# Optimization experiments

Hardware: AMD Instinct MI355X
Metric: run time of the kernel (lower is better)

## Reference

```python
import jax, jax.numpy as jnp
import numpy as np

B, S, D, H = 2, 2048, 4096, 16
HD = D // H          # 256 head dim
ROT = 64             # rotary_dim
MASK_FILL = -65504.0 # fp16 min, as in the IPEX kernel


def _sinusoidal_positions(num_pos, dim):
    inv_freq = 1.0 / (10000.0 ** (np.arange(0, dim, 2, dtype=np.float32) / dim))
    sinusoid = np.einsum('i,j->ij', np.arange(num_pos, dtype=np.float32), inv_freq)
    return np.concatenate([np.sin(sinusoid), np.cos(sinusoid)], axis=-1).astype(np.float32)  # [num_pos, dim]


def setup_inputs() -> dict:
    key = jax.random.key(0)
    ks = jax.random.split(key, 6)
    w = 0.02
    return {
        'hidden_states': jax.random.normal(ks[0], (B, S, D), jnp.float32),
        'Wq': jax.random.normal(ks[1], (D, D), jnp.float32) * w,
        'Wk': jax.random.normal(ks[2], (D, D), jnp.float32) * w,
        'Wv': jax.random.normal(ks[3], (D, D), jnp.float32) * w,
        'Wo': jax.random.normal(ks[4], (D, D), jnp.float32) * w,
        'embed_positions': jnp.asarray(_sinusoidal_positions(S, ROT)),  # [max_pos, ROT] sin|cos
        'attention_mask': jnp.zeros((B, 1, 1, S), jnp.float32),
        'position_ids': jnp.tile(jnp.arange(S, dtype=jnp.int32), (B, 1)),
    }


def rotate_every_two(x):
    x1 = x[..., ::2]
    x2 = x[..., 1::2]
    return jnp.stack((-x2, x1), axis=-1).reshape(x.shape)


def reference(hidden_states, Wq, Wk, Wv, Wo, embed_positions, attention_mask, position_ids):
    b, s, d = hidden_states.shape
    q = (hidden_states @ Wq).reshape(b, s, H, HD)
    k = (hidden_states @ Wk).reshape(b, s, H, HD)
    v = (hidden_states @ Wv).reshape(b, s, H, HD)

    # gather sin/cos per position, GPT-J interleaved layout
    sincos = embed_positions[position_ids]            # [b, s, ROT]
    sin, cos = jnp.split(sincos, 2, axis=-1)          # each [b, s, ROT/2]
    sin = jnp.repeat(sin, 2, axis=-1)[:, :, None, :]  # [b, s, 1, ROT]
    cos = jnp.repeat(cos, 2, axis=-1)[:, :, None, :]

    def rope(t):
        tr = t[..., :ROT]
        tr = tr * cos + rotate_every_two(tr) * sin
        return jnp.concatenate([tr, t[..., ROT:]], axis=-1)

    q = rope(q).transpose(0, 2, 1, 3)  # [b, H, s, HD]
    k = rope(k).transpose(0, 2, 1, 3)
    v = v.transpose(0, 2, 1, 3)

    scores = jnp.einsum('bhqd,bhkd->bhqk', q, k)
    causal = jnp.tril(jnp.ones((s, s), bool))
    # IPEX order: mask-fill with -65504 BEFORE dividing by sqrt(head_dim)
    scores = jnp.where(causal, scores, MASK_FILL) / jnp.sqrt(jnp.float32(HD))
    scores = scores + attention_mask
    attn = jax.nn.softmax(scores, axis=-1)

    out = jnp.einsum('bhqk,bhkd->bhqd', attn, v)
    out = out.transpose(0, 2, 1, 3).reshape(b, s, d)
    return out @ Wo
```

## Files before the change

### kernel.cpp

```cpp
#include <hip/hip_runtime.h>

typedef __bf16 bf16x8 __attribute__((ext_vector_type(8)));
typedef float f32x4 __attribute__((ext_vector_type(4)));
typedef unsigned short u16;
typedef unsigned int u32;
typedef u16 u16x8 __attribute__((ext_vector_type(8)));
typedef u16 u16x4 __attribute__((ext_vector_type(4)));

#define DEVI __device__ __forceinline__

static constexpr size_t R_ELEMS = (size_t)4096 * 4096;

DEVI u16 f2bf(float f) {
  u32 x = __float_as_uint(f);
  u32 r = x + 0x7FFFu + ((x >> 16) & 1u);
  return (u16)(r >> 16);
}
DEVI float bf2f(u16 u) { return __uint_as_float(((u32)u) << 16); }

#define GLOAD_LDS16(gp, lp)                                                     \
  __builtin_amdgcn_global_load_lds(                                             \
      (const __attribute__((address_space(1))) void*)(gp),                      \
      (__attribute__((address_space(3))) void*)(lp), 16, 0, 0)

#define MFMA16(a, b, c) __builtin_amdgcn_mfma_f32_16x16x32_bf16((a), (b), (c), 0, 0, 0)

__global__ void k_cvt(const float* __restrict__ in, u16* __restrict__ out, int n8) {
  int i = blockIdx.x * blockDim.x + threadIdx.x;
  if (i >= n8) return;
  const float4* p = (const float4*)in + (size_t)i * 2;
  float4 a = p[0], b = p[1];
  u16x8 o;
  o[0] = f2bf(a.x); o[1] = f2bf(a.y); o[2] = f2bf(a.z); o[3] = f2bf(a.w);
  o[4] = f2bf(b.x); o[5] = f2bf(b.y); o[6] = f2bf(b.z); o[7] = f2bf(b.w);
  *((u16x8*)out + i) = o;
}

__global__ void k_transpose_w(const float* __restrict__ W, u16* __restrict__ Wt) {
  __shared__ float t[64][65];
  int kb = blockIdx.x * 64, nb = blockIdx.y * 64;
  int tx = threadIdx.x, ty = threadIdx.y;
#pragma unroll
  for (int i = 0; i < 16; i++) {
    int r = i * 4 + ty;
    t[r][tx] = W[(size_t)(kb + r) * 4096 + nb + tx];
  }
  __syncthreads();
#pragma unroll
  for (int i = 0; i < 16; i++) {
    int r = i * 4 + ty;
    Wt[(size_t)(nb + r) * 4096 + kb + tx] = f2bf(t[tx][r]);
  }
}

template <int OUTMODE>
__global__ __launch_bounds__(256, 2) void k_gemm(const u16* __restrict__ A,
                                                 const u16* __restrict__ Bt,
                                                 void* __restrict__ outp) {
  __shared__ __attribute__((aligned(16))) u16 lA[128 * 64];
  __shared__ __attribute__((aligned(16))) u16 lB[256 * 64];
  const int tid = threadIdx.x;
  const int w = tid >> 6, lane = tid & 63;
  const int wr = w >> 1, wc = w & 1;
  const int m0 = blockIdx.y * 128, n0 = blockIdx.x * 256;

  f32x4 acc[4][8];
#pragma unroll
  for (int i = 0; i < 4; i++)
#pragma unroll
    for (int j = 0; j < 8; j++) acc[i][j] = (f32x4){0.f, 0.f, 0.f, 0.f};

  const int srow = lane >> 3;
  const int scol = ((lane & 7) ^ srow) * 8;
  const u16* Abase = A + (size_t)(m0 + w * 32 + srow) * 4096 + scol;
  const u16* Bbase = Bt + (size_t)(n0 + w * 64 + srow) * 4096 + scol;
  u16* lAw = lA + w * 2048;
  u16* lBw = lB + w * 4096;

  const int lm = lane & 15;
  const int lk = lane >> 4;
  const int swz = (lane & 7) << 3;

  for (int kt = 0; kt < 64; ++kt) {
    __syncthreads();
#pragma unroll
    for (int i = 0; i < 4; ++i)
      GLOAD_LDS16(Abase + (size_t)kt * 64 + (size_t)i * 8 * 4096, lAw + i * 512);
#pragma unroll
    for (int i = 0; i < 8; ++i)
      GLOAD_LDS16(Bbase + (size_t)kt * 64 + (size_t)i * 8 * 4096, lBw + i * 512);
    __syncthreads();
#pragma unroll
    for (int ks = 0; ks < 2; ++ks) {
      bf16x8 af[4], bfr[8];
      const int ce = (ks * 32 + lk * 8) ^ swz;
#pragma unroll
      for (int mi = 0; mi < 4; mi++)
        af[mi] = *(const bf16x8*)(lA + (wr * 64 + mi * 16 + lm) * 64 + ce);
#pragma unroll
      for (int ni = 0; ni < 8; ni++)
        bfr[ni] = *(const bf16x8*)(lB + (wc * 128 + ni * 16 + lm) * 64 + ce);
#pragma unroll
      for (int mi = 0; mi < 4; mi++)
#pragma unroll
        for (int ni = 0; ni < 8; ni++)
          acc[mi][ni] = MFMA16(af[mi], bfr[ni], acc[mi][ni]);
    }
  }

#pragma unroll
  for (int mi = 0; mi < 4; mi++) {
#pragma unroll
    for (int ni = 0; ni < 8; ni++) {
      const int mb = m0 + wr * 64 + mi * 16 + lk * 4;
      const int n = n0 + wc * 128 + ni * 16 + lm;
      if (OUTMODE == 2) {
        u16x4 vt;
#pragma unroll
        for (int r = 0; r < 4; r++) vt[r] = f2bf(acc[mi][ni][r]);
        u16* o = (u16*)outp;
        *(u16x4*)&o[(size_t)((mb >> 11) * 16 + ((n >> 8) & 15)) * 524288 +
                    (size_t)(n & 255) * 2048 + (mb & 2047)] = vt;
      } else {
        float* o = (float*)outp;
#pragma unroll
        for (int r = 0; r < 4; r++) o[(size_t)(mb + r) * 4096 + n] = acc[mi][ni][r];
      }
    }
  }
}

__global__ __launch_bounds__(256, 2) void k_gemm_qk(const u16* __restrict__ A,
                                                    const u16* __restrict__ Btq,
                                                    const u16* __restrict__ Btk,
                                                    const float* __restrict__ ep,
                                                    const int* __restrict__ pid,
                                                    u16* __restrict__ Qo,
                                                    u16* __restrict__ Ko) {
  __shared__ __attribute__((aligned(16))) u16 lA[128 * 64];
  __shared__ __attribute__((aligned(16))) u16 lBq[128 * 64];
  __shared__ __attribute__((aligned(16))) u16 lBk[128 * 64];
  const int tid = threadIdx.x;
  const int w = tid >> 6, lane = tid & 63;
  const int wr = w >> 1, wc = w & 1;
  const int m0 = blockIdx.y * 128, n0 = blockIdx.x * 128;

  f32x4 accq[4][4], acck[4][4];
#pragma unroll
  for (int i = 0; i < 4; i++)
#pragma unroll
    for (int j = 0; j < 4; j++) {
      accq[i][j] = (f32x4){0.f, 0.f, 0.f, 0.f};
      acck[i][j] = (f32x4){0.f, 0.f, 0.f, 0.f};
    }

  const int srow = lane >> 3;
  const int scol = ((lane & 7) ^ srow) * 8;
  const u16* Abase = A + (size_t)(m0 + w * 32 + srow) * 4096 + scol;
  const u16* Bqb = Btq + (size_t)(n0 + w * 32 + srow) * 4096 + scol;
  const u16* Bkb = Btk + (size_t)(n0 + w * 32 + srow) * 4096 + scol;
  u16* lAw = lA + w * 2048;
  u16* lBqw = lBq + w * 2048;
  u16* lBkw = lBk + w * 2048;

  const int lm = lane & 15;
  const int lk = lane >> 4;
  const int swz = (lane & 7) << 3;

  for (int kt = 0; kt < 64; ++kt) {
    __syncthreads();
#pragma unroll
    for (int i = 0; i < 4; ++i) {
      GLOAD_LDS16(Abase + (size_t)kt * 64 + (size_t)i * 8 * 4096, lAw + i * 512);
      GLOAD_LDS16(Bqb + (size_t)kt * 64 + (size_t)i * 8 * 4096, lBqw + i * 512);
      GLOAD_LDS16(Bkb + (size_t)kt * 64 + (size_t)i * 8 * 4096, lBkw + i * 512);
    }
    __syncthreads();
#pragma unroll
    for (int ks = 0; ks < 2; ++ks) {
      bf16x8 af[4], bfr[4];
      const int ce = (ks * 32 + lk * 8) ^ swz;
#pragma unroll
      for (int mi = 0; mi < 4; mi++)
        af[mi] = *(const bf16x8*)(lA + (wr * 64 + mi * 16 + lm) * 64 + ce);
#pragma unroll
      for (int ni = 0; ni < 4; ni++)
        bfr[ni] = *(const bf16x8*)(lBq + (wc * 64 + ni * 16 + lm) * 64 + ce);
#pragma unroll
      for (int mi = 0; mi < 4; mi++)
#pragma unroll
        for (int ni = 0; ni < 4; ni++)
          accq[mi][ni] = MFMA16(af[mi], bfr[ni], accq[mi][ni]);
#pragma unroll
      for (int ni = 0; ni < 4; ni++)
        bfr[ni] = *(const bf16x8*)(lBk + (wc * 64 + ni * 16 + lm) * 64 + ce);
#pragma unroll
      for (int mi = 0; mi < 4; mi++)
#pragma unroll
        for (int ni = 0; ni < 4; ni++)
          acck[mi][ni] = MFMA16(af[mi], bfr[ni], acck[mi][ni]);
    }
  }

  const bool ropew = ((blockIdx.x & 1) == 0) && (wc == 0);
  if (ropew) {
#pragma unroll
    for (int mi = 0; mi < 4; mi++) {
#pragma unroll
      for (int r = 0; r < 4; r++) {
        const int m = m0 + wr * 64 + mi * 16 + lk * 4 + r;
        const int pos = pid[(m >> 11) * 2048 + (m & 2047)];
#pragma unroll
        for (int ni = 0; ni < 4; ni++) {
          const int p = (ni * 16 + lm) >> 1;
          const float sn = ep[pos * 64 + p];
          const float cs = ep[pos * 64 + 32 + p];
          float q = accq[mi][ni][r], k = acck[mi][ni][r];
          float qp = __shfl_xor(q, 1, 64), kp = __shfl_xor(k, 1, 64);
          accq[mi][ni][r] = (lm & 1) ? (q * cs + qp * sn) : (q * cs - qp * sn);
          acck[mi][ni][r] = (lm & 1) ? (k * cs + kp * sn) : (k * cs - kp * sn);
        }
      }
    }
  }

#pragma unroll
  for (int mi = 0; mi < 4; mi++) {
#pragma unroll
    for (int ni = 0; ni < 4; ni++) {
#pragma unroll
      for (int r = 0; r < 4; r++) {
        int m = m0 + wr * 64 + mi * 16 + lk * 4 + r;
        int n = n0 + wc * 64 + ni * 16 + lm;
        size_t idx = (size_t)((m >> 11) * 16 + ((n >> 8) & 15)) * 524288 +
                     (size_t)(m & 2047) * 256 + (n & 255);
        Qo[idx] = f2bf(accq[mi][ni][r]);
        Ko[idx] = f2bf(acck[mi][ni][r]);
      }
    }
  }
}

__global__ __launch_bounds__(512, 2) void k_attn(const u16* __restrict__ Q,
                                                 const u16* __restrict__ K,
                                                 const u16* __restrict__ Vt,
                                                 const float* __restrict__ amask,
                                                 u16* __restrict__ AO) {
  __shared__ __attribute__((aligned(16))) u16 lK[2][64 * 256];
  __shared__ __attribute__((aligned(16))) u16 lV[2][256 * 64];
  __shared__ __attribute__((aligned(16))) u16 lP[8][16 * 64];

  const int tid = threadIdx.x, w = tid >> 6, lane = tid & 63;
  const int wg = blockIdx.x;
  const int bh = wg & 31;
  const int qt = (wg < 256) ? (15 - (wg >> 5)) : ((wg - 256) >> 5);
  const int b = bh >> 4;
  const int lm = lane & 15, lk = lane >> 4;
  const size_t head = (size_t)bh * (2048 * 256);
  const int q0 = qt * 128 + w * 16;
  const int swzl = (lane & 7) << 3;

  const int kreg_row = (lane >> 5);
  const int kcol = (lane & 31) * 8;
  const int vreg_row = (lane >> 3);
  const int vcol = (lane & 7) * 8;

#define ASTAGE(t)                                                                \
  {                                                                              \
    const int bb_ = (t) & 1;                                                     \
    const int kv0_ = (t) * 64;                                                   \
    _Pragma("unroll") for (int i_ = 0; i_ < 4; i_++) {                           \
      const int reg_ = w + i_ * 8;                                               \
      const int krow_ = reg_ * 2 + kreg_row;                                     \
      GLOAD_LDS16(K + head + (size_t)(kv0_ + krow_) * 256 +                      \
                      (kcol ^ ((krow_ & 7) << 3)),                               \
                  &lK[bb_][reg_ * 512 + lane * 8]);                              \
      const int vrow_ = reg_ * 8 + vreg_row;                                     \
      GLOAD_LDS16(Vt + head + (size_t)vrow_ * 2048 + kv0_ +                      \
                      (vcol ^ ((vrow_ & 7) << 3)),                               \
                  &lV[bb_][reg_ * 512 + lane * 8]);                              \
    }                                                                            \
  }

  bf16x8 qf[8];
#pragma unroll
  for (int c = 0; c < 8; c++)
    qf[c] = *(const bf16x8*)(Q + head + (size_t)(q0 + lm) * 256 + c * 32 + lk * 8);

  f32x4 o[16];
#pragma unroll
  for (int i = 0; i < 16; i++) o[i] = (f32x4){0.f, 0.f, 0.f, 0.f};
  float m_s = -__builtin_inff();
  float l_s = 0.f;

  const int ntiles = 2 * qt + 2;
  ASTAGE(0);

  for (int t = 0; t < ntiles; ++t) {
    const int kv0 = t * 64;
    const int bb = t & 1;
    float4 amq[4];
#pragma unroll
    for (int kb = 0; kb < 4; kb++)
      amq[kb] = *(const float4*)(amask + b * 2048 + kv0 + kb * 16 + lk * 4);
    if (t + 1 < ntiles) {
      ASTAGE(t + 1);
      asm volatile("s_waitcnt vmcnt(8)" ::: "memory");
    } else {
      asm volatile("s_waitcnt vmcnt(0)" ::: "memory");
    }
    __builtin_amdgcn_s_barrier();

    if (q0 + 15 >= kv0) {
      const u16* lKb = lK[bb];
      const u16* lVb = lV[bb];

      float sx[4][4];
      __builtin_amdgcn_s_setprio(1);
#pragma unroll
      for (int kb = 0; kb < 4; kb++) {
        f32x4 sa = (f32x4){0.f, 0.f, 0.f, 0.f};
        const int kvr = kb * 16 + lm;
#pragma unroll
        for (int c = 0; c < 8; c++) {
          bf16x8 kf = *(const bf16x8*)(lKb + kvr * 256 + ((c * 32 + lk * 8) ^ swzl));
          sa = __builtin_amdgcn_mfma_f32_16x16x32_bf16(kf, qf[c], sa, 0, 0, 0);
        }
#pragma unroll
        for (int r = 0; r < 4; r++)
          sx[kb][r] = sa[r] * 0.0625f + ((const float*)&amq[kb])[r];
      }
      __builtin_amdgcn_s_setprio(0);

      const int q_abs = q0 + lm;
      float tm = -__builtin_inff();
#pragma unroll
      for (int kb = 0; kb < 4; kb++)
#pragma unroll
        for (int r = 0; r < 4; r++) {
          bool valid = (kv0 + kb * 16 + lk * 4 + r) <= q_abs;
          tm = fmaxf(tm, valid ? sx[kb][r] : -__builtin_inff());
        }
      tm = fmaxf(tm, __shfl_xor(tm, 16, 64));
      tm = fmaxf(tm, __shfl_xor(tm, 32, 64));

      if (!__all(tm <= m_s + 8.0f)) {
        float mnew = fmaxf(m_s, tm);
        float alpha = __expf(m_s - mnew);
        m_s = mnew;
        l_s *= alpha;
        float af0 = __shfl(alpha, lk * 4 + 0, 64);
        float af1 = __shfl(alpha, lk * 4 + 1, 64);
        float af2 = __shfl(alpha, lk * 4 + 2, 64);
        float af3 = __shfl(alpha, lk * 4 + 3, 64);
#pragma unroll
        for (int dblk = 0; dblk < 16; dblk++) {
          o[dblk][0] *= af0; o[dblk][1] *= af1;
          o[dblk][2] *= af2; o[dblk][3] *= af3;
        }
      }

      float psum = 0.f;
#pragma unroll
      for (int kb = 0; kb < 4; kb++) {
        u16x4 ph;
#pragma unroll
        for (int r = 0; r < 4; r++) {
          bool valid = (kv0 + kb * 16 + lk * 4 + r) <= q_abs;
          float p = valid ? __expf(sx[kb][r] - m_s) : 0.f;
          psum += p;
          ph[r] = f2bf(p);
        }
        *(u16x4*)(&lP[w][lm * 64 + ((kb * 16 + lk * 4) ^ swzl)]) = ph;
      }
      psum += __shfl_xor(psum, 16, 64);
      psum += __shfl_xor(psum, 32, 64);
      l_s += psum;

      bf16x8 pa[2];
#pragma unroll
      for (int kh = 0; kh < 2; kh++)
        pa[kh] = *(const bf16x8*)(&lP[w][lm * 64 + ((lk * 8 + kh * 32) ^ swzl)]);
      __builtin_amdgcn_s_setprio(1);
#pragma unroll
      for (int dblk = 0; dblk < 16; dblk++) {
        const int dr = dblk * 16 + lm;
#pragma unroll
        for (int kh = 0; kh < 2; kh++) {
          bf16x8 vf = *(const bf16x8*)(lVb + dr * 64 + ((lk * 8 + kh * 32) ^ swzl));
          o[dblk] = __builtin_amdgcn_mfma_f32_16x16x32_bf16(pa[kh], vf, o[dblk], 0, 0, 0);
        }
      }
      __builtin_amdgcn_s_setprio(0);
    }
    __builtin_amdgcn_s_barrier();
  }
#undef ASTAGE

  float linv[4];
#pragma unroll
  for (int r = 0; r < 4; r++) linv[r] = 1.0f / __shfl(l_s, lk * 4 + r, 64);
#pragma unroll
  for (int r = 0; r < 4; r++) {
    const int s_abs = q0 + lk * 4 + r;
#pragma unroll
    for (int dblk = 0; dblk < 16; dblk++) {
      int d = (bh & 15) * 256 + dblk * 16 + lm;
      AO[((size_t)b * 2048 + s_abs) * 4096 + d] = f2bf(o[dblk][r] * linv[r]);
    }
  }
}

extern "C" void kernel_launch(void* const* d_in, const int* in_sizes, int n_in,
                              void* d_out, int out_size, void* d_ws, size_t ws_size,
                              hipStream_t stream) {
  (void)in_sizes; (void)n_in; (void)out_size; (void)ws_size;
  const float* hs = (const float*)d_in[0];
  const float* Wq = (const float*)d_in[1];
  const float* Wk = (const float*)d_in[2];
  const float* Wv = (const float*)d_in[3];
  const float* Wo = (const float*)d_in[4];
  const float* ep = (const float*)d_in[5];
  const float* am = (const float*)d_in[6];
  const int* pid = (const int*)d_in[7];

  u16* r0 = (u16*)d_ws;
  u16* r1 = r0 + R_ELEMS;
  u16* r2 = r1 + R_ELEMS;
  u16* r3 = r2 + R_ELEMS;
  u16* r4 = r3 + R_ELEMS;
  float* out = (float*)d_out;

  dim3 b256(256), b512(512), bT(64, 4);
  k_cvt<<<dim3(8192), b256, 0, stream>>>(hs, r0, 16777216 / 8);

  k_transpose_w<<<dim3(64, 64), bT, 0, stream>>>(Wq, r1);
  k_transpose_w<<<dim3(64, 64), bT, 0, stream>>>(Wk, r2);
  k_gemm_qk<<<dim3(32, 32), b256, 0, stream>>>(r0, r1, r2, ep, pid, r3, r4);

  k_transpose_w<<<dim3(64, 64), bT, 0, stream>>>(Wv, r1);
  k_gemm<2><<<dim3(16, 32), b256, 0, stream>>>(r0, r1, r2);

  k_attn<<<dim3(512), b512, 0, stream>>>(r3, r4, r2, am, r0);

  k_transpose_w<<<dim3(64, 64), bT, 0, stream>>>(Wo, r1);
  k_gemm<1><<<dim3(16, 32), b256, 0, stream>>>(r0, r1, out);
}
```

Baseline: 702.4 us.

## Give each attention wave two query sub-tiles and drop K/V double buffering

The attention kernel drops to 256 threads per block, with each wave owning 32 query rows as two 16-row sub-tiles. Each K/V fragment read from LDS now feeds two MFMAs, which halves LDS read traffic per unit of math. The K/V staging goes from double-buffered to single-buffered, so each block needs far less LDS and two blocks can fit per CU. The cost is that global loads no longer overlap compute inside a block, register pressure rises with twice the accumulators and Q fragments, and causal skipping now works at 32-row rather than 16-row granularity.

Result: slower. 867.9 us (+23.6%).

```diff
diff --git a/kernel.cpp b/kernel.cpp
--- a/kernel.cpp
+++ b/kernel.cpp
@@ -241,14 +241,14 @@
   }
 }
 
-__global__ __launch_bounds__(512, 2) void k_attn(const u16* __restrict__ Q,
+__global__ __launch_bounds__(256, 2) void k_attn(const u16* __restrict__ Q,
                                                  const u16* __restrict__ K,
                                                  const u16* __restrict__ Vt,
                                                  const float* __restrict__ amask,
                                                  u16* __restrict__ AO) {
-  __shared__ __attribute__((aligned(16))) u16 lK[2][64 * 256];
-  __shared__ __attribute__((aligned(16))) u16 lV[2][256 * 64];
-  __shared__ __attribute__((aligned(16))) u16 lP[8][16 * 64];
+  __shared__ __attribute__((aligned(16))) u16 lK[64 * 256];
+  __shared__ __attribute__((aligned(16))) u16 lV[256 * 64];
+  __shared__ __attribute__((aligned(16))) u16 lP[4][2][16 * 64];
 
   const int tid = threadIdx.x, w = tid >> 6, lane = tid & 63;
   const int wg = blockIdx.x;
@@ -257,7 +257,7 @@
   const int b = bh >> 4;
   const int lm = lane & 15, lk = lane >> 4;
   const size_t head = (size_t)bh * (2048 * 256);
-  const int q0 = qt * 128 + w * 16;
+  const int q0 = qt * 128 + w * 32;
   const int swzl = (lane & 7) << 3;
 
   const int kreg_row = (lane >> 5);
@@ -267,128 +267,134 @@
 
 #define ASTAGE(t)                                                                \
   {                                                                              \
-    const int bb_ = (t) & 1;                                                     \
     const int kv0_ = (t) * 64;                                                   \
-    _Pragma("unroll") for (int i_ = 0; i_ < 4; i_++) {                           \
-      const int reg_ = w + i_ * 8;                                               \
+    _Pragma("unroll") for (int i_ = 0; i_ < 8; i_++) {                           \
+      const int reg_ = w + i_ * 4;                                               \
       const int krow_ = reg_ * 2 + kreg_row;                                     \
       GLOAD_LDS16(K + head + (size_t)(kv0_ + krow_) * 256 +                      \
                       (kcol ^ ((krow_ & 7) << 3)),                               \
-                  &lK[bb_][reg_ * 512 + lane * 8]);                              \
+                  &lK[reg_ * 512 + lane * 8]);                                   \
       const int vrow_ = reg_ * 8 + vreg_row;                                     \
       GLOAD_LDS16(Vt + head + (size_t)vrow_ * 2048 + kv0_ +                      \
                       (vcol ^ ((vrow_ & 7) << 3)),                               \
-                  &lV[bb_][reg_ * 512 + lane * 8]);                              \
+                  &lV[reg_ * 512 + lane * 8]);                                   \
     }                                                                            \
   }
 
-  bf16x8 qf[8];
-#pragma unroll
-  for (int c = 0; c < 8; c++)
-    qf[c] = *(const bf16x8*)(Q + head + (size_t)(q0 + lm) * 256 + c * 32 + lk * 8);
-
-  f32x4 o[16];
-#pragma unroll
-  for (int i = 0; i < 16; i++) o[i] = (f32x4){0.f, 0.f, 0.f, 0.f};
-  float m_s = -__builtin_inff();
-  float l_s = 0.f;
+  bf16x8 qf[2][8];
+#pragma unroll
+  for (int j = 0; j < 2; j++)
+#pragma unroll
+    for (int c = 0; c < 8; c++)
+      qf[j][c] = *(const bf16x8*)(Q + head + (size_t)(q0 + j * 16 + lm) * 256 +
+                                  c * 32 + lk * 8);
+
+  f32x4 o[2][16];
+#pragma unroll
+  for (int j = 0; j < 2; j++)
+#pragma unroll
+    for (int i = 0; i < 16; i++) o[j][i] = (f32x4){0.f, 0.f, 0.f, 0.f};
+  float m2[2] = {-__builtin_inff(), -__builtin_inff()};
+  float l2[2] = {0.f, 0.f};
 
   const int ntiles = 2 * qt + 2;
-  ASTAGE(0);
 
   for (int t = 0; t < ntiles; ++t) {
     const int kv0 = t * 64;
-    const int bb = t & 1;
     float4 amq[4];
 #pragma unroll
     for (int kb = 0; kb < 4; kb++)
       amq[kb] = *(const float4*)(amask + b * 2048 + kv0 + kb * 16 + lk * 4);
-    if (t + 1 < ntiles) {
-      ASTAGE(t + 1);
-      asm volatile("s_waitcnt vmcnt(8)" ::: "memory");
-    } else {
-      asm volatile("s_waitcnt vmcnt(0)" ::: "memory");
-    }
+    ASTAGE(t);
+    asm volatile("s_waitcnt vmcnt(0)" ::: "memory");
     __builtin_amdgcn_s_barrier();
 
-    if (q0 + 15 >= kv0) {
-      const u16* lKb = lK[bb];
-      const u16* lVb = lV[bb];
-
-      float sx[4][4];
+    if (q0 + 31 >= kv0) {
+      float sx[2][4][4];
       __builtin_amdgcn_s_setprio(1);
 #pragma unroll
       for (int kb = 0; kb < 4; kb++) {
-        f32x4 sa = (f32x4){0.f, 0.f, 0.f, 0.f};
+        f32x4 sa0 = (f32x4){0.f, 0.f, 0.f, 0.f};
+        f32x4 sa1 = (f32x4){0.f, 0.f, 0.f, 0.f};
         const int kvr = kb * 16 + lm;
 #pragma unroll
         for (int c = 0; c < 8; c++) {
-          bf16x8 kf = *(const bf16x8*)(lKb + kvr * 256 + ((c * 32 + lk * 8) ^ swzl));
-          sa = __builtin_amdgcn_mfma_f32_16x16x32_bf16(kf, qf[c], sa, 0, 0, 0);
-        }
-#pragma unroll
-        for (int r = 0; r < 4; r++)
-          sx[kb][r] = sa[r] * 0.0625f + ((const float*)&amq[kb])[r];
+          bf16x8 kf = *(const bf16x8*)(lK + kvr * 256 + ((c * 32 + lk * 8) ^ swzl));
+          sa0 = MFMA16(kf, qf[0][c], sa0);
+          sa1 = MFMA16(kf, qf[1][c], sa1);
+        }
+#pragma unroll
+        for (int r = 0; r < 4; r++) {
+          sx[0][kb][r] = sa0[r] * 0.0625f + ((const float*)&amq[kb])[r];
+          sx[1][kb][r] = sa1[r] * 0.0625f + ((const float*)&amq[kb])[r];
+        }
       }
       __builtin_amdgcn_s_setprio(0);
 
-      const int q_abs = q0 + lm;
-      float tm = -__builtin_inff();
-#pragma unroll
-      for (int kb = 0; kb < 4; kb++)
-#pragma unroll
-        for (int r = 0; r < 4; r++) {
-          bool valid = (kv0 + kb * 16 + lk * 4 + r) <= q_abs;
-          tm = fmaxf(tm, valid ? sx[kb][r] : -__builtin_inff());
-        }
-      tm = fmaxf(tm, __shfl_xor(tm, 16, 64));
-      tm = fmaxf(tm, __shfl_xor(tm, 32, 64));
-
-      if (!__all(tm <= m_s + 8.0f)) {
-        float mnew = fmaxf(m_s, tm);
-        float alpha = __expf(m_s - mnew);
-        m_s = mnew;
-        l_s *= alpha;
-        float af0 = __shfl(alpha, lk * 4 + 0, 64);
-        float af1 = __shfl(alpha, lk * 4 + 1, 64);
-        float af2 = __shfl(alpha, lk * 4 + 2, 64);
-        float af3 = __shfl(alpha, lk * 4 + 3, 64);
-#pragma unroll
-        for (int dblk = 0; dblk < 16; dblk++) {
-          o[dblk][0] *= af0; o[dblk][1] *= af1;
-          o[dblk][2] *= af2; o[dblk][3] *= af3;
-        }
-      }
-
-      float psum = 0.f;
-#pragma unroll
-      for (int kb = 0; kb < 4; kb++) {
-        u16x4 ph;
-#pragma unroll
-        for (int r = 0; r < 4; r++) {
-          bool valid = (kv0 + kb * 16 + lk * 4 + r) <= q_abs;
-          float p = valid ? __expf(sx[kb][r] - m_s) : 0.f;
-          psum += p;
-          ph[r] = f2bf(p);
-        }
-        *(u16x4*)(&lP[w][lm * 64 + ((kb * 16 + lk * 4) ^ swzl)]) = ph;
-      }
-      psum += __shfl_xor(psum, 16, 64);
-      psum += __shfl_xor(psum, 32, 64);
-      l_s += psum;
-
-      bf16x8 pa[2];
-#pragma unroll
-      for (int kh = 0; kh < 2; kh++)
-        pa[kh] = *(const bf16x8*)(&lP[w][lm * 64 + ((lk * 8 + kh * 32) ^ swzl)]);
+#pragma unroll
+      for (int j = 0; j < 2; j++) {
+        const int q_abs = q0 + j * 16 + lm;
+        float tm = -__builtin_inff();
+#pragma unroll
+        for (int kb = 0; kb < 4; kb++)
+#pragma unroll
+          for (int r = 0; r < 4; r++) {
+            bool valid = (kv0 + kb * 16 + lk * 4 + r) <= q_abs;
+            tm = fmaxf(tm, valid ? sx[j][kb][r] : -__builtin_inff());
+          }
+        tm = fmaxf(tm, __shfl_xor(tm, 16, 64));
+        tm = fmaxf(tm, __shfl_xor(tm, 32, 64));
+
+        if (!__all(tm <= m2[j] + 8.0f)) {
+          float mnew = fmaxf(m2[j], tm);
+          float alpha = __expf(m2[j] - mnew);
+          m2[j] = mnew;
+          l2[j] *= alpha;
+          float af0 = __shfl(alpha, lk * 4 + 0, 64);
+          float af1 = __shfl(alpha, lk * 4 + 1, 64);
+          float af2 = __shfl(alpha, lk * 4 + 2, 64);
+          float af3 = __shfl(alpha, lk * 4 + 3, 64);
+#pragma unroll
+          for (int dblk = 0; dblk < 16; dblk++) {
+            o[j][dblk][0] *= af0; o[j][dblk][1] *= af1;
+            o[j][dblk][2] *= af2; o[j][dblk][3] *= af3;
+          }
+        }
+
+        float psum = 0.f;
+#pragma unroll
+        for (int kb = 0; kb < 4; kb++) {
+          u16x4 ph;
+#pragma unroll
+          for (int r = 0; r < 4; r++) {
+            bool valid = (kv0 + kb * 16 + lk * 4 + r) <= q_abs;
+            float p = valid ? __expf(sx[j][kb][r] - m2[j]) : 0.f;
+            psum += p;
+            ph[r] = f2bf(p);
+          }
+          *(u16x4*)(&lP[w][j][lm * 64 + ((kb * 16 + lk * 4) ^ swzl)]) = ph;
+        }
+        psum += __shfl_xor(psum, 16, 64);
+        psum += __shfl_xor(psum, 32, 64);
+        l2[j] += psum;
+      }
+
+      bf16x8 pa[2][2];
+#pragma unroll
+      for (int j = 0; j < 2; j++)
+#pragma unroll
+        for (int kh = 0; kh < 2; kh++)
+          pa[j][kh] =
+              *(const bf16x8*)(&lP[w][j][lm * 64 + ((lk * 8 + kh * 32) ^ swzl)]);
       __builtin_amdgcn_s_setprio(1);
 #pragma unroll
       for (int dblk = 0; dblk < 16; dblk++) {
         const int dr = dblk * 16 + lm;
 #pragma unroll
         for (int kh = 0; kh < 2; kh++) {
-          bf16x8 vf = *(const bf16x8*)(lVb + dr * 64 + ((lk * 8 + kh * 32) ^ swzl));
-          o[dblk] = __builtin_amdgcn_mfma_f32_16x16x32_bf16(pa[kh], vf, o[dblk], 0, 0, 0);
+          bf16x8 vf = *(const bf16x8*)(lV + dr * 64 + ((lk * 8 + kh * 32) ^ swzl));
+          o[0][dblk] = MFMA16(pa[0][kh], vf, o[0][dblk]);
+          o[1][dblk] = MFMA16(pa[1][kh], vf, o[1][dblk]);
         }
       }
       __builtin_amdgcn_s_setprio(0);
@@ -397,16 +403,19 @@
   }
 #undef ASTAGE
 
-  float linv[4];
-#pragma unroll
-  for (int r = 0; r < 4; r++) linv[r] = 1.0f / __shfl(l_s, lk * 4 + r, 64);
-#pragma unroll
-  for (int r = 0; r < 4; r++) {
-    const int s_abs = q0 + lk * 4 + r;
-#pragma unroll
-    for (int dblk = 0; dblk < 16; dblk++) {
-      int d = (bh & 15) * 256 + dblk * 16 + lm;
-      AO[((size_t)b * 2048 + s_abs) * 4096 + d] = f2bf(o[dblk][r] * linv[r]);
+#pragma unroll
+  for (int j = 0; j < 2; j++) {
+    float linv[4];
+#pragma unroll
+    for (int r = 0; r < 4; r++) linv[r] = 1.0f / __shfl(l2[j], lk * 4 + r, 64);
+#pragma unroll
+    for (int r = 0; r < 4; r++) {
+      const int s_abs = q0 + j * 16 + lk * 4 + r;
+#pragma unroll
+      for (int dblk = 0; dblk < 16; dblk++) {
+        int d = (bh & 15) * 256 + dblk * 16 + lm;
+        AO[((size_t)b * 2048 + s_abs) * 4096 + d] = f2bf(o[j][dblk][r] * linv[r]);
+      }
     }
   }
 }
@@ -431,7 +440,7 @@
   u16* r4 = r3 + R_ELEMS;
   float* out = (float*)d_out;
 
-  dim3 b256(256), b512(512), bT(64, 4);
+  dim3 b256(256), bT(64, 4);
   k_cvt<<<dim3(8192), b256, 0, stream>>>(hs, r0, 16777216 / 8);
 
   k_transpose_w<<<dim3(64, 64), bT, 0, stream>>>(Wq, r1);
@@ -441,7 +450,7 @@
   k_transpose_w<<<dim3(64, 64), bT, 0, stream>>>(Wv, r1);
   k_gemm<2><<<dim3(16, 32), b256, 0, stream>>>(r0, r1, r2);
 
-  k_attn<<<dim3(512), b512, 0, stream>>>(r3, r4, r2, am, r0);
+  k_attn<<<dim3(512), b256, 0, stream>>>(r3, r4, r2, am, r0);
 
   k_transpose_w<<<dim3(64, 64), bT, 0, stream>>>(Wo, r1);
   k_gemm<1><<<dim3(16, 32), b256, 0, stream>>>(r0, r1, out);
```
